# Optimization experiments

Measured on AMD Instinct MI355X. Metric: run time of the kernel, lower is better.

Reference implementation:

```python
import jax, jax.numpy as jnp
import numpy as np

B, NT, DIM, H = 8, 1024, 768, 12
HD = DIM // H
SCALE = HD ** -0.5


def setup_inputs() -> dict:
    key = jax.random.key(0)
    ks = jax.random.split(key, 9)
    s = DIM ** -0.5
    return {
        "tfeat": jax.random.normal(ks[0], (B, NT, DIM), jnp.float32),
        "wq": jax.random.normal(ks[1], (DIM, DIM), jnp.float32) * s,
        "bq": jnp.zeros((DIM,), jnp.float32),
        "wk": jax.random.normal(ks[2], (DIM, DIM), jnp.float32) * s,
        "bk": jnp.zeros((DIM,), jnp.float32),
        "wv": jax.random.normal(ks[3], (DIM, DIM), jnp.float32) * s,
        "bv": jnp.zeros((DIM,), jnp.float32),
        "wp": jax.random.normal(ks[4], (DIM, DIM), jnp.float32) * s,
        "bp": jnp.zeros((DIM,), jnp.float32),
    }


def reference(tfeat, wq, bq, wk, bk, wv, bv, wp, bp):
    # Linear stores weight [out, in]; y = x @ W^T + b
    def split_heads(x):  # [B,Nt,C] -> [B,H,Nt,hd]
        b, n, c = x.shape
        return x.reshape(b, n, H, HD).transpose(0, 2, 1, 3)

    q = split_heads(tfeat @ wq.T + bq)
    k = split_heads(tfeat @ wk.T + bk)
    v = split_heads(tfeat @ wv.T + bv)
    # [B,H,Nt,Nt]
    attn = jax.nn.softmax(jnp.einsum('bhqd,bhkd->bhqk', q, k) * SCALE, axis=-1)
    # dropout is identity in eval mode
    x = jnp.einsum('bhqk,bhkd->bhqd', attn, v)
    x = x.transpose(0, 2, 1, 3).reshape(tfeat.shape)
    x = x @ wp.T + bp
    return (x, attn)
```

## Files before the change

kernel.cpp:

```cpp
#include <hip/hip_runtime.h>
#include <math.h>

#define B_    8
#define NT_   1024
#define DIM_  768
#define H_    12
#define HD_   64
#define SCALE_ 0.125f
#define T_ELEMS 6291456UL

typedef _Float16 half8  __attribute__((ext_vector_type(8)));
typedef _Float16 half4v __attribute__((ext_vector_type(4)));
typedef float    floatx4 __attribute__((ext_vector_type(4)));

#if __has_builtin(__builtin_amdgcn_exp2f)
#define EXP2F(x) __builtin_amdgcn_exp2f(x)
#else
#define EXP2F(x) exp2f(x)
#endif

#define GLD16(gp, lp) __builtin_amdgcn_global_load_lds( \
    (const __attribute__((address_space(1))) unsigned int*)(gp), \
    (__attribute__((address_space(3))) unsigned int*)(lp), 16, 0, 0)

__global__ void cvt4(const float* __restrict__ in, _Float16* __restrict__ out,
                     int n4) {
  int i = blockIdx.x * 256 + threadIdx.x;
  if (i < n4) {
    float4 v = ((const float4*)in)[i];
    half4v h = { (_Float16)v.x, (_Float16)v.y, (_Float16)v.z, (_Float16)v.w };
    *(half4v*)(out + 4 * (size_t)i) = h;
  }
}

template<int MODE>
__global__ __launch_bounds__(256) void gemm128(
    const _Float16* __restrict__ A, const _Float16* __restrict__ Bt,
    const float* __restrict__ b0_, const float* __restrict__ b1_,
    const float* __restrict__ b2_, _Float16* __restrict__ outh,
    float* __restrict__ outf, int K)
{
  __shared__ _Float16 As[128 * 32];
  __shared__ _Float16 Bs[128 * 32];
  const int t    = threadIdx.x;
  const int w    = t >> 6, lane = t & 63;
  const int quad = lane >> 4, l16 = lane & 15;
  const int wm   = (w >> 1) * 64, wn = (w & 1) * 64;

  const int nbx = gridDim.x;
  int lin = blockIdx.y * nbx + blockIdx.x;
  const int cpx = (nbx * gridDim.y) >> 3;
  lin = (lin & 7) * cpx + (lin >> 3);
  const int m0 = (lin % nbx) * 128, n0 = (lin / nbx) * 128;

  const _Float16* gA = A  + (size_t)(m0 + (t >> 2)) * K + (t & 3) * 8;
  const _Float16* gB = Bt + (size_t)(n0 + (t >> 2)) * K + (t & 3) * 8;
  _Float16* lA = As + w * 512;
  _Float16* lB = Bs + w * 512;
  const size_t rowK = (size_t)64 * K;

  floatx4 acc[4][4] = {};

  for (int k0 = 0; k0 < K; k0 += 32) {
    __syncthreads();
    GLD16(gA + k0,        lA);
    GLD16(gA + rowK + k0, lA + 2048);
    GLD16(gB + k0,        lB);
    GLD16(gB + rowK + k0, lB + 2048);
    __syncthreads();

    half8 af[4], bf[4];
#pragma unroll
    for (int i = 0; i < 4; i++)
      af[i] = *(const half8*)(As + (wm + i * 16 + l16) * 32 + quad * 8);
#pragma unroll
    for (int j = 0; j < 4; j++)
      bf[j] = *(const half8*)(Bs + (wn + j * 16 + l16) * 32 + quad * 8);
#pragma unroll
    for (int i = 0; i < 4; i++)
#pragma unroll
      for (int j = 0; j < 4; j++)
        acc[i][j] = __builtin_amdgcn_mfma_f32_16x16x32_f16(af[i], bf[j],
                                                           acc[i][j], 0, 0, 0);
  }

  const int sel = (MODE == 0) ? (n0 / 768) : 0;
  const float* bb = (MODE == 0)
                      ? (sel == 0 ? b0_ : (sel == 1 ? b1_ : b2_))
                      : b0_;
#pragma unroll
  for (int j = 0; j < 4; j++) {
    const int col = n0 + wn + j * 16 + l16;
    const int cl  = col - sel * 768;
    const float bv = bb[cl];
#pragma unroll
    for (int i = 0; i < 4; i++)
#pragma unroll
      for (int r = 0; r < 4; r++) {
        const int row = m0 + wm + i * 16 + quad * 4 + r;
        const float v = acc[i][j][r] + bv;
        if (MODE == 0)
          outh[(size_t)sel * T_ELEMS + (size_t)row * 768 + cl] = (_Float16)v;
        else
          outf[(size_t)row * 768 + col] = v;
      }
  }
}

__global__ __launch_bounds__(256) void transpose_v(
    const _Float16* __restrict__ Vh, _Float16* __restrict__ VT)
{
  __shared__ _Float16 tile[64][72];
  const int t = threadIdx.x;
  const int tt = blockIdx.x, h = blockIdx.y, b = blockIdx.z;
  const int lrow = t >> 2, lcol = (t & 3) * 16;

  const _Float16* src = Vh + ((size_t)b * NT_ + tt * 64 + lrow) * DIM_ + h * HD_;
  *(uint4*)(&tile[lrow][lcol])     = *(const uint4*)(src + lcol);
  *(uint4*)(&tile[lrow][lcol + 8]) = *(const uint4*)(src + lcol + 8);
  __syncthreads();

  alignas(16) _Float16 vh[16];
#pragma unroll
  for (int c = 0; c < 16; c++) vh[c] = tile[lcol + c][lrow];
  _Float16* dst = VT + ((size_t)(b * H_ + h) * HD_ + lrow) * NT_ + tt * 64 + lcol;
  *(uint4*)(dst)     = *(const uint4*)(vh);
  *(uint4*)(dst + 8) = *(const uint4*)(vh + 8);
}

__global__ __launch_bounds__(256) void attn_kernel(
    const _Float16* __restrict__ Qh, const _Float16* __restrict__ Kh,
    const _Float16* __restrict__ VT, float* __restrict__ attn_out,
    _Float16* __restrict__ Xh)
{
  __shared__ _Float16 Ps[64][72];

  const int t    = threadIdx.x;
  const int w    = t >> 6, lane = t & 63;
  const int quad = lane >> 4, l16 = lane & 15;

  const int bid  = blockIdx.x;
  const int slot = bid & 7, i = bid >> 3;
  const int g    = slot + 8 * (i >> 4);
  const int qt   = i & 15;
  const int b    = g / H_, h = g % H_;
  const int q0   = qt * 64;

  const _Float16* Qb = Qh + ((size_t)b * NT_) * DIM_ + h * HD_;
  const _Float16* Kb = Kh + ((size_t)b * NT_) * DIM_ + h * HD_;
  const _Float16* Vb = VT + (size_t)g * HD_ * NT_;

  half8 qf[2];
  {
    const _Float16* qr = Qb + (size_t)(q0 + w * 16 + l16) * DIM_ + quad * 8;
    qf[0] = *(const half8*)(qr);
    qf[1] = *(const half8*)(qr + 32);
  }

  const float C2 = 0.18033688011112042f;

  float lsum[4] = {0.f, 0.f, 0.f, 0.f};
  for (int kt = 0; kt < 16; kt++) {
    const _Float16* kb = Kb + (size_t)(kt * 64 + l16) * DIM_ + quad * 8;
    floatx4 s[4] = {};
#pragma unroll
    for (int ks = 0; ks < 2; ks++)
#pragma unroll
      for (int j = 0; j < 4; j++) {
        half8 bk = *(const half8*)(kb + (size_t)(j * 16) * DIM_ + ks * 32);
        s[j] = __builtin_amdgcn_mfma_f32_16x16x32_f16(qf[ks], bk, s[j], 0, 0, 0);
      }
#pragma unroll
    for (int j = 0; j < 4; j++)
#pragma unroll
      for (int r = 0; r < 4; r++)
        lsum[r] += EXP2F(s[j][r] * C2);
  }

  float mb[4];
#pragma unroll
  for (int r = 0; r < 4; r++) {
    float ts = lsum[r];
    for (int off = 1; off < 16; off <<= 1) ts += __shfl_xor(ts, off, 64);
    mb[r] = log2f(ts);
  }

  floatx4 oacc[4] = {};
  float* attn_b = attn_out + ((size_t)g * NT_ + q0) * NT_;

  for (int kt = 0; kt < 16; kt++) {
    const _Float16* kb = Kb + (size_t)(kt * 64 + l16) * DIM_ + quad * 8;
    floatx4 s[4] = {};
#pragma unroll
    for (int ks = 0; ks < 2; ks++)
#pragma unroll
      for (int j = 0; j < 4; j++) {
        half8 bk = *(const half8*)(kb + (size_t)(j * 16) * DIM_ + ks * 32);
        s[j] = __builtin_amdgcn_mfma_f32_16x16x32_f16(qf[ks], bk, s[j], 0, 0, 0);
      }

    half8 bv[2][4];
    const _Float16* vb = Vb + (size_t)l16 * NT_ + kt * 64 + quad * 8;
#pragma unroll
    for (int ks = 0; ks < 2; ks++)
#pragma unroll
      for (int j2 = 0; j2 < 4; j2++)
        bv[ks][j2] = *(const half8*)(vb + (size_t)(j2 * 16) * NT_ + ks * 32);

#pragma unroll
    for (int j = 0; j < 4; j++)
#pragma unroll
      for (int r = 0; r < 4; r++) {
        const float p = EXP2F(fmaf(s[j][r], C2, -mb[r]));
        const int qr = w * 16 + quad * 4 + r;
        attn_b[(size_t)qr * NT_ + kt * 64 + j * 16 + l16] = p;
        Ps[qr][j * 16 + l16] = (_Float16)p;
      }

#pragma unroll
    for (int ks = 0; ks < 2; ks++) {
      half8 pa = *(const half8*)(&Ps[w * 16 + l16][ks * 32 + quad * 8]);
#pragma unroll
      for (int j2 = 0; j2 < 4; j2++)
        oacc[j2] = __builtin_amdgcn_mfma_f32_16x16x32_f16(pa, bv[ks][j2],
                                                          oacc[j2], 0, 0, 0);
    }
  }

#pragma unroll
  for (int j2 = 0; j2 < 4; j2++)
#pragma unroll
    for (int r = 0; r < 4; r++) {
      const int qr = q0 + w * 16 + quad * 4 + r;
      Xh[((size_t)b * NT_ + qr) * DIM_ + h * HD_ + j2 * 16 + l16] = (_Float16)oacc[j2][r];
    }
}

extern "C" void kernel_launch(void* const* d_in, const int* in_sizes, int n_in,
                              void* d_out, int out_size, void* d_ws, size_t ws_size,
                              hipStream_t stream) {
  const float* tfeat = (const float*)d_in[0];
  const float* wq    = (const float*)d_in[1];
  const float* bq    = (const float*)d_in[2];
  const float* wk    = (const float*)d_in[3];
  const float* bk    = (const float*)d_in[4];
  const float* wv    = (const float*)d_in[5];
  const float* bv    = (const float*)d_in[6];
  const float* wp    = (const float*)d_in[7];
  const float* bp    = (const float*)d_in[8];
  float* out = (float*)d_out;

  const size_t T = T_ELEMS;
  const size_t W = (size_t)DIM_ * DIM_;

  _Float16* ws  = (_Float16*)d_ws;
  _Float16* tfh = ws;
  _Float16* wqh = ws + T;
  _Float16* wkh = ws + T + W;
  _Float16* wvh = ws + T + 2 * W;
  _Float16* wph = ws + T + 3 * W;
  _Float16* Qh  = ws + T + 4 * W;
  _Float16* Kh  = Qh + T;
  _Float16* Vh  = Kh + T;
  _Float16* Xh  = Vh + T;
  _Float16* VTt = Xh + T;

  cvt4<<<(int)(T / 4 / 256), 256, 0, stream>>>(tfeat, tfh, (int)(T / 4));
  cvt4<<<(int)(W / 4 / 256), 256, 0, stream>>>(wq, wqh, (int)(W / 4));
  cvt4<<<(int)(W / 4 / 256), 256, 0, stream>>>(wk, wkh, (int)(W / 4));
  cvt4<<<(int)(W / 4 / 256), 256, 0, stream>>>(wv, wvh, (int)(W / 4));
  cvt4<<<(int)(W / 4 / 256), 256, 0, stream>>>(wp, wph, (int)(W / 4));

  gemm128<0><<<dim3(64, 18), 256, 0, stream>>>(tfh, wqh, bq, bk, bv, Qh, nullptr, 768);

  transpose_v<<<dim3(16, 12, 8), 256, 0, stream>>>(Vh, VTt);

  attn_kernel<<<1536, 256, 0, stream>>>(Qh, Kh, VTt, out + T, Xh);

  gemm128<1><<<dim3(64, 6), 256, 0, stream>>>(Xh, wph, bp, nullptr, nullptr, nullptr, out, 768);
}
```

Before: 762.6 us.

## Stage K tiles through swizzled double-buffered LDS in attention; merge weight conversions

The attention kernel now copies each 64-row K tile into double-buffered LDS using global_load_lds with an XOR swizzle. All four waves share the tile instead of each wave reading K straight from global memory, and the next tile's load overlaps the current compute. The attn probability stores and the Xh stores become nontemporal, and the four weight fp32→fp16 conversions are merged into one launch. The GEMM's XCD-aware block remapping is removed, and a __syncthreads is added per K iteration, which may cost some L2 locality and add sync overhead.

```diff
diff --git a/kernel.cpp b/kernel.cpp
--- a/kernel.cpp
+++ b/kernel.cpp
@@ -6,7 +6,6 @@
 #define DIM_  768
 #define H_    12
 #define HD_   64
-#define SCALE_ 0.125f
 #define T_ELEMS 6291456UL
 
 typedef _Float16 half8  __attribute__((ext_vector_type(8)));
@@ -22,6 +21,8 @@
 #define GLD16(gp, lp) __builtin_amdgcn_global_load_lds( \
     (const __attribute__((address_space(1))) unsigned int*)(gp), \
     (__attribute__((address_space(3))) unsigned int*)(lp), 16, 0, 0)
+
+#define MFMA16(a, b, c) __builtin_amdgcn_mfma_f32_16x16x32_f16((a), (b), (c), 0, 0, 0)
 
 __global__ void cvt4(const float* __restrict__ in, _Float16* __restrict__ out,
                      int n4) {
@@ -31,6 +32,18 @@
     half4v h = { (_Float16)v.x, (_Float16)v.y, (_Float16)v.z, (_Float16)v.w };
     *(half4v*)(out + 4 * (size_t)i) = h;
   }
+}
+
+__global__ void cvtW4(const float* __restrict__ w0, const float* __restrict__ w1,
+                      const float* __restrict__ w2, const float* __restrict__ w3,
+                      _Float16* __restrict__ out) {
+  const int n4 = (DIM_ * DIM_) / 4;
+  int i = blockIdx.x * 256 + threadIdx.x;
+  const int seg = i / n4, off = i - seg * n4;
+  const float* src = (seg == 0) ? w0 : (seg == 1) ? w1 : (seg == 2) ? w2 : w3;
+  float4 v = ((const float4*)src)[off];
+  half4v h = { (_Float16)v.x, (_Float16)v.y, (_Float16)v.z, (_Float16)v.w };
+  *(half4v*)(out + 4 * (size_t)i) = h;
 }
 
 template<int MODE>
@@ -46,12 +59,7 @@
   const int w    = t >> 6, lane = t & 63;
   const int quad = lane >> 4, l16 = lane & 15;
   const int wm   = (w >> 1) * 64, wn = (w & 1) * 64;
-
-  const int nbx = gridDim.x;
-  int lin = blockIdx.y * nbx + blockIdx.x;
-  const int cpx = (nbx * gridDim.y) >> 3;
-  lin = (lin & 7) * cpx + (lin >> 3);
-  const int m0 = (lin % nbx) * 128, n0 = (lin / nbx) * 128;
+  const int m0   = blockIdx.x * 128, n0 = blockIdx.y * 128;
 
   const _Float16* gA = A  + (size_t)(m0 + (t >> 2)) * K + (t & 3) * 8;
   const _Float16* gB = Bt + (size_t)(n0 + (t >> 2)) * K + (t & 3) * 8;
@@ -80,8 +88,7 @@
     for (int i = 0; i < 4; i++)
 #pragma unroll
       for (int j = 0; j < 4; j++)
-        acc[i][j] = __builtin_amdgcn_mfma_f32_16x16x32_f16(af[i], bf[j],
-                                                           acc[i][j], 0, 0, 0);
+        acc[i][j] = MFMA16(af[i], bf[j], acc[i][j]);
   }
 
   const int sel = (MODE == 0) ? (n0 / 768) : 0;
@@ -133,6 +140,7 @@
     const _Float16* __restrict__ VT, float* __restrict__ attn_out,
     _Float16* __restrict__ Xh)
 {
+  __shared__ _Float16 Ks[2 * 4096];
   __shared__ _Float16 Ps[64][72];
 
   const int t    = threadIdx.x;
@@ -150,6 +158,20 @@
   const _Float16* Kb = Kh + ((size_t)b * NT_) * DIM_ + h * HD_;
   const _Float16* Vb = VT + (size_t)g * HD_ * NT_;
 
+  const int krl   = (w << 3) + (lane >> 3);
+  const int kgran = (lane & 7) ^ (lane >> 3);
+  const _Float16* Kstage = Kb + (size_t)krl * DIM_ + kgran * 8;
+  _Float16* kdst = Ks + (w << 9);
+
+#define STAGE_K(kt, c) do { \
+    const _Float16* s_ = Kstage + (size_t)(kt) * 64 * DIM_; \
+    GLD16(s_,                     kdst + (c) * 4096); \
+    GLD16(s_ + (size_t)32 * DIM_, kdst + (c) * 4096 + 2048); \
+  } while (0)
+
+  const int rsw0 = ((quad      ^ (l16 & 7)) << 3);
+  const int rsw1 = (((4 + quad) ^ (l16 & 7)) << 3);
+
   half8 qf[2];
   {
     const _Float16* qr = Qb + (size_t)(q0 + w * 16 + l16) * DIM_ + quad * 8;
@@ -160,21 +182,27 @@
   const float C2 = 0.18033688011112042f;
 
   float lsum[4] = {0.f, 0.f, 0.f, 0.f};
+  STAGE_K(0, 0);
+  __syncthreads();
   for (int kt = 0; kt < 16; kt++) {
-    const _Float16* kb = Kb + (size_t)(kt * 64 + l16) * DIM_ + quad * 8;
+    const int cur = kt & 1;
+    if (kt < 15) STAGE_K(kt + 1, cur ^ 1);
+    const _Float16* kb = Ks + cur * 4096;
     floatx4 s[4] = {};
 #pragma unroll
-    for (int ks = 0; ks < 2; ks++)
-#pragma unroll
-      for (int j = 0; j < 4; j++) {
-        half8 bk = *(const half8*)(kb + (size_t)(j * 16) * DIM_ + ks * 32);
-        s[j] = __builtin_amdgcn_mfma_f32_16x16x32_f16(qf[ks], bk, s[j], 0, 0, 0);
-      }
+    for (int j = 0; j < 4; j++) {
+      const int rb = (j * 16 + l16) * 64;
+      half8 k0 = *(const half8*)(kb + rb + rsw0);
+      half8 k1 = *(const half8*)(kb + rb + rsw1);
+      s[j] = MFMA16(qf[0], k0, s[j]);
+      s[j] = MFMA16(qf[1], k1, s[j]);
+    }
 #pragma unroll
     for (int j = 0; j < 4; j++)
 #pragma unroll
       for (int r = 0; r < 4; r++)
         lsum[r] += EXP2F(s[j][r] * C2);
+    __syncthreads();
   }
 
   float mb[4];
@@ -188,16 +216,11 @@
   floatx4 oacc[4] = {};
   float* attn_b = attn_out + ((size_t)g * NT_ + q0) * NT_;
 
+  STAGE_K(0, 0);
+  __syncthreads();
   for (int kt = 0; kt < 16; kt++) {
-    const _Float16* kb = Kb + (size_t)(kt * 64 + l16) * DIM_ + quad * 8;
-    floatx4 s[4] = {};
-#pragma unroll
-    for (int ks = 0; ks < 2; ks++)
-#pragma unroll
-      for (int j = 0; j < 4; j++) {
-        half8 bk = *(const half8*)(kb + (size_t)(j * 16) * DIM_ + ks * 32);
-        s[j] = __builtin_amdgcn_mfma_f32_16x16x32_f16(qf[ks], bk, s[j], 0, 0, 0);
-      }
+    const int cur = kt & 1;
+    if (kt < 15) STAGE_K(kt + 1, cur ^ 1);
 
     half8 bv[2][4];
     const _Float16* vb = Vb + (size_t)l16 * NT_ + kt * 64 + quad * 8;
@@ -206,6 +229,17 @@
 #pragma unroll
       for (int j2 = 0; j2 < 4; j2++)
         bv[ks][j2] = *(const half8*)(vb + (size_t)(j2 * 16) * NT_ + ks * 32);
+
+    const _Float16* kb = Ks + cur * 4096;
+    floatx4 s[4] = {};
+#pragma unroll
+    for (int j = 0; j < 4; j++) {
+      const int rb = (j * 16 + l16) * 64;
+      half8 k0 = *(const half8*)(kb + rb + rsw0);
+      half8 k1 = *(const half8*)(kb + rb + rsw1);
+      s[j] = MFMA16(qf[0], k0, s[j]);
+      s[j] = MFMA16(qf[1], k1, s[j]);
+    }
 
 #pragma unroll
     for (int j = 0; j < 4; j++)
@@ -213,7 +247,7 @@
       for (int r = 0; r < 4; r++) {
         const float p = EXP2F(fmaf(s[j][r], C2, -mb[r]));
         const int qr = w * 16 + quad * 4 + r;
-        attn_b[(size_t)qr * NT_ + kt * 64 + j * 16 + l16] = p;
+        __builtin_nontemporal_store(p, &attn_b[(size_t)qr * NT_ + kt * 64 + j * 16 + l16]);
         Ps[qr][j * 16 + l16] = (_Float16)p;
       }
 
@@ -222,9 +256,9 @@
       half8 pa = *(const half8*)(&Ps[w * 16 + l16][ks * 32 + quad * 8]);
 #pragma unroll
       for (int j2 = 0; j2 < 4; j2++)
-        oacc[j2] = __builtin_amdgcn_mfma_f32_16x16x32_f16(pa, bv[ks][j2],
-                                                          oacc[j2], 0, 0, 0);
+        oacc[j2] = MFMA16(pa, bv[ks][j2], oacc[j2]);
     }
+    __syncthreads();
   }
 
 #pragma unroll
@@ -232,8 +266,10 @@
 #pragma unroll
     for (int r = 0; r < 4; r++) {
       const int qr = q0 + w * 16 + quad * 4 + r;
-      Xh[((size_t)b * NT_ + qr) * DIM_ + h * HD_ + j2 * 16 + l16] = (_Float16)oacc[j2][r];
+      __builtin_nontemporal_store((_Float16)oacc[j2][r],
+          &Xh[((size_t)b * NT_ + qr) * DIM_ + h * HD_ + j2 * 16 + l16]);
     }
+#undef STAGE_K
 }
 
 extern "C" void kernel_launch(void* const* d_in, const int* in_sizes, int n_in,
@@ -256,8 +292,6 @@
   _Float16* ws  = (_Float16*)d_ws;
   _Float16* tfh = ws;
   _Float16* wqh = ws + T;
-  _Float16* wkh = ws + T + W;
-  _Float16* wvh = ws + T + 2 * W;
   _Float16* wph = ws + T + 3 * W;
   _Float16* Qh  = ws + T + 4 * W;
   _Float16* Kh  = Qh + T;
@@ -266,10 +300,7 @@
   _Float16* VTt = Xh + T;
 
   cvt4<<<(int)(T / 4 / 256), 256, 0, stream>>>(tfeat, tfh, (int)(T / 4));
-  cvt4<<<(int)(W / 4 / 256), 256, 0, stream>>>(wq, wqh, (int)(W / 4));
-  cvt4<<<(int)(W / 4 / 256), 256, 0, stream>>>(wk, wkh, (int)(W / 4));
-  cvt4<<<(int)(W / 4 / 256), 256, 0, stream>>>(wv, wvh, (int)(W / 4));
-  cvt4<<<(int)(W / 4 / 256), 256, 0, stream>>>(wp, wph, (int)(W / 4));
+  cvtW4<<<(int)(4 * W / 4 / 256), 256, 0, stream>>>(wq, wk, wv, wp, wqh);
 
   gemm128<0><<<dim3(64, 18), 256, 0, stream>>>(tfh, wqh, bq, bk, bv, Qh, nullptr, 768);
 
```

Result: faster. 625.5 us (-18.0%).
